# Performance work log

Measured on AMD Instinct MI355X. Metric: run time of the kernel, lower is better.

Reference implementation:

```python
import jax, jax.numpy as jnp
import numpy as np

H = 64       # hidden size hard-coded in the module
NH = 4       # n_heads
S = 500      # stock_num
D = 10       # num_day
T = 40       # num_text (news per day)
FP = 3       # price features
FT = 512     # text embedding dim


def gru_scan(x, Wih, Whh, bih, bhh):
    """Single-sequence GRU (torch gate convention). x: (T, F) -> hidden states (T, H)."""
    gi = x @ Wih + bih  # (T, 3H) precompute input gates outside the scan

    def step(h, g):
        gh = h @ Whh + bhh
        r = jax.nn.sigmoid(g[:H] + gh[:H])
        z = jax.nn.sigmoid(g[H:2 * H] + gh[H:2 * H])
        n = jnp.tanh(g[2 * H:] + r * gh[2 * H:])
        h_new = (1.0 - z) * n + z * h
        return h_new, h_new

    h0 = jnp.zeros((H,), x.dtype)
    _, hs = jax.lax.scan(step, h0, gi)
    return hs


def attn_pool(hs, W, v):
    """Additive attention pooling over time. hs: (T, H) -> (H,)."""
    scores = jnp.tanh(hs @ W) @ v          # (T,)
    alpha = jax.nn.softmax(scores)
    return alpha @ hs


def _gru_params(key, fin, scale=0.08):
    k1, k2, k3, k4 = jax.random.split(key, 4)
    return (jax.random.normal(k1, (S, fin, 3 * H)) * scale,
            jax.random.normal(k2, (S, H, 3 * H)) * scale,
            jax.random.normal(k3, (S, 3 * H)) * scale,
            jax.random.normal(k4, (S, 3 * H)) * scale)


def _attn_params(key, scale=0.08):
    k1, k2 = jax.random.split(key)
    return (jax.random.normal(k1, (S, H, H)) * scale,
            jax.random.normal(k2, (S, H)) * scale)


def setup_inputs() -> dict:
    key = jax.random.key(0)
    ks = jax.random.split(key, 20)
    inp = {}
    inp['text_input'] = jax.random.normal(ks[0], (S, D, T, FT), dtype=jnp.float32)
    inp['price_input'] = jax.random.normal(ks[1], (S, D, FP), dtype=jnp.float32)
    inp['label'] = jax.random.randint(ks[2], (S,), 0, 2)
    inp['adj'] = jnp.ones((S, S), dtype=jnp.float32)
    inp['train'] = 0
    # per-stock stacked parameters
    (inp['Wih_p'], inp['Whh_p'], inp['bih_p'], inp['bhh_p']) = _gru_params(ks[3], FP)
    (inp['Wa_p'], inp['va_p']) = _attn_params(ks[4])
    (inp['Wih_t'], inp['Whh_t'], inp['bih_t'], inp['bhh_t']) = _gru_params(ks[5], FT)
    (inp['Wa_t'], inp['va_t']) = _attn_params(ks[6])
    (inp['Wih_s'], inp['Whh_s'], inp['bih_s'], inp['bhh_s']) = _gru_params(ks[7], H)
    (inp['Wa_s'], inp['va_s']) = _attn_params(ks[8])
    inp['Wb'] = jax.random.normal(ks[9], (S, H, H, H)) * 0.05   # Bilinear weight (out,in1,in2)
    inp['bb'] = jax.random.normal(ks[10], (S, H)) * 0.05
    inp['Wbl'] = jax.random.normal(ks[11], (S, H, 2)) * 0.08
    inp['bbl'] = jax.random.normal(ks[12], (S, 2)) * 0.08
    # shared cross-stock self-attention projections and final fc
    inp['Wq'] = jax.random.normal(ks[13], (H, H)) * 0.08
    inp['bq'] = jax.random.normal(ks[14], (H,)) * 0.08
    inp['Wk'] = jax.random.normal(ks[15], (H, H)) * 0.08
    inp['bk'] = jax.random.normal(ks[16], (H,)) * 0.08
    inp['Wf'] = jax.random.normal(ks[17], (H, 2)) * 0.08
    inp['bf'] = jax.random.normal(ks[18], (2,)) * 0.08
    return inp


def _forward(text_input, price_input, label,
             Wih_p, Whh_p, bih_p, bhh_p, Wa_p, va_p,
             Wih_t, Whh_t, bih_t, bhh_t, Wa_t, va_t,
             Wih_s, Whh_s, bih_s, bhh_s, Wa_s, va_s,
             Wb, bb, Wbl, bbl, Wq, bq, Wk, bk, Wf, bf):
    # ---- per-stock price encoder: GRU over days + attention pooling ----
    def enc_price(x, a, b, c, d, W, v):
        return attn_pool(gru_scan(x, a, b, c, d), W, v)
    x_price = jax.vmap(enc_price)(price_input, Wih_p, Whh_p, bih_p, bhh_p, Wa_p, va_p)  # (S, H)

    # ---- per-stock, per-day text encoder ----
    def enc_text_stock(xdays, a, b, c, d, W, v):
        return jax.vmap(lambda x: attn_pool(gru_scan(x, a, b, c, d), W, v))(xdays)  # (D, H)
    news = jax.vmap(enc_text_stock)(text_input, Wih_t, Whh_t, bih_t, bhh_t, Wa_t, va_t)  # (S, D, H)

    # ---- per-stock sequence encoder over days ----
    text_vec = jax.vmap(enc_price)(news, Wih_s, Whh_s, bih_s, bhh_s, Wa_s, va_s)  # (S, H)

    # ---- bilinear fusion: tanh(Bilinear(text, price)) ----
    combined = jnp.tanh(jnp.einsum('si,skij,sj->sk', text_vec, Wb, x_price) + bb)  # (S, H)

    # ---- per-stock blending head ----
    out_1 = jnp.tanh(jnp.einsum('si,sik->sk', combined, Wbl) + bbl)  # (S, 2)

    # ---- cross-stock multi-head self-attention (q,k projected, v identity) ----
    dh = H // NH
    q = (combined @ Wq + bq).reshape(S, NH, dh)
    k = (combined @ Wk + bk).reshape(S, NH, dh)
    v = combined.reshape(S, NH, dh)
    scores = jnp.einsum('shd,thd->hst', q, k) / (dh ** 0.5)
    attn = jax.nn.softmax(scores, axis=-1)
    attn_out = jnp.einsum('hst,thd->shd', attn, v).reshape(S, H)

    x = jax.nn.elu(attn_out @ Wf + bf)  # (S, 2)
    output = jax.nn.softmax(x + out_1, axis=1)
    # faithful to the original: CrossEntropyLoss applied to already-softmaxed output
    logp = jax.nn.log_softmax(output, axis=1)
    loss = -jnp.mean(logp[jnp.arange(S), label])
    return loss, output


def reference(text_input, price_input, label, adj, train,
              Wih_p, Whh_p, bih_p, bhh_p, Wa_p, va_p,
              Wih_t, Whh_t, bih_t, bhh_t, Wa_t, va_t,
              Wih_s, Whh_s, bih_s, bhh_s, Wa_s, va_s,
              Wb, bb, Wbl, bbl, Wq, bq, Wk, bk, Wf, bf):
    return _forward(text_input, price_input, label,
                    Wih_p, Whh_p, bih_p, bhh_p, Wa_p, va_p,
                    Wih_t, Whh_t, bih_t, bhh_t, Wa_t, va_t,
                    Wih_s, Whh_s, bih_s, bhh_s, Wa_s, va_s,
                    Wb, bb, Wbl, bbl, Wq, bq, Wk, bk, Wf, bf)
```

## Files before the change

### kernel.cpp

```cpp
#include <hip/hip_runtime.h>

#define Sn 500
#define Dn 10
#define Tn 40
#define FPn 3
#define FTn 512
#define Hn 64
#define G3 192
#define NHn 4

typedef __attribute__((ext_vector_type(8))) short bf8_t;
typedef __attribute__((ext_vector_type(4))) float f4_t;

__device__ __forceinline__ unsigned short f2bf(float f) {
    union { float f; unsigned int u; } v; v.f = f;
    unsigned int r = v.u + 0x7fffu + ((v.u >> 16) & 1u);
    return (unsigned short)(r >> 16);
}
__device__ __forceinline__ float bflo(unsigned int u) {
    union { unsigned int u; float f; } v; v.u = u << 16; return v.f;
}
__device__ __forceinline__ float bfhi(unsigned int u) {
    union { unsigned int u; float f; } v; v.u = u & 0xffff0000u; return v.f;
}
__device__ __forceinline__ unsigned int cvtpk(float lo, float hi) {
    unsigned int r;
    asm("v_cvt_pk_bf16_f32 %0, %1, %2" : "=v"(r) : "v"(lo), "v"(hi));
    return r;
}
__device__ __forceinline__ float sigmoidf_(float x) { return 1.f / (1.f + __expf(-x)); }
__device__ __forceinline__ float tanhf_(float x) {
    x = fminf(15.f, fmaxf(-15.f, x));
    float e = __expf(2.f * x);
    return (e - 1.f) / (e + 1.f);
}
__device__ __forceinline__ float dot8(uint4 wv, f4_t hA, f4_t hB) {
    return bflo(wv.x) * hA[0] + bfhi(wv.x) * hA[1]
         + bflo(wv.y) * hA[2] + bfhi(wv.y) * hA[3]
         + bflo(wv.z) * hB[0] + bfhi(wv.z) * hB[1]
         + bflo(wv.w) * hB[2] + bfhi(wv.w) * hB[3];
}
union bfu { bf8_t v; unsigned int u[4]; };

__global__ __launch_bounds__(256, 2) void gi_gemm4(
    const float* __restrict__ text, const float* __restrict__ Wih,
    const float* __restrict__ bih, float* __restrict__ gi2)
{
    const int bid = blockIdx.x;
    const int xcd = bid & 7, ix = bid >> 3;
    const int swz = (xcd < 4 ? xcd * 313 : 4 * 313 + (xcd - 4) * 312) + ix;
    const int s = swz / 5, fi = swz % 5;
    const int tid = threadIdx.x, w = tid >> 6, l = tid & 63;
    const int lr = l & 15, kg = l >> 4;

    const float* Wihs = Wih + (size_t)s * FTn * G3 + w * 48 + lr;
    const float* xrow = text + ((size_t)s * 400 + fi * 80 + lr) * FTn + kg * 8;

    f4_t acc[5][3];
    #pragma unroll
    for (int a = 0; a < 5; a++)
        #pragma unroll
        for (int b = 0; b < 3; b++) acc[a][b] = (f4_t){0.f, 0.f, 0.f, 0.f};

    f4_t an0[5], an1[5];
    #pragma unroll
    for (int mt = 0; mt < 5; ++mt) {
        const float* p = xrow + (size_t)mt * 16 * FTn;
        an0[mt] = *(const f4_t*)p; an1[mt] = *(const f4_t*)(p + 4);
    }

    for (int kk = 0; kk < 16; ++kk) {
        bfu af[5];
        #pragma unroll
        for (int mt = 0; mt < 5; ++mt) {
            af[mt].u[0] = cvtpk(an0[mt][0], an0[mt][1]);
            af[mt].u[1] = cvtpk(an0[mt][2], an0[mt][3]);
            af[mt].u[2] = cvtpk(an1[mt][0], an1[mt][1]);
            af[mt].u[3] = cvtpk(an1[mt][2], an1[mt][3]);
        }
        if (kk < 15) {
            const float* px = xrow + (kk + 1) * 32;
            #pragma unroll
            for (int mt = 0; mt < 5; ++mt) {
                const float* p = px + (size_t)mt * 16 * FTn;
                an0[mt] = *(const f4_t*)p; an1[mt] = *(const f4_t*)(p + 4);
            }
        }
        bfu bfr[3];
        const float* bp0 = Wihs + (size_t)(kk * 32 + kg * 8) * G3;
        #pragma unroll
        for (int nc = 0; nc < 3; ++nc) {
            const float* bp = bp0 + nc * 16;
            float b0 = bp[0], b1 = bp[G3], b2 = bp[2 * G3], b3 = bp[3 * G3];
            float b4 = bp[4 * G3], b5 = bp[5 * G3], b6 = bp[6 * G3], b7 = bp[7 * G3];
            bfr[nc].u[0] = cvtpk(b0, b1); bfr[nc].u[1] = cvtpk(b2, b3);
            bfr[nc].u[2] = cvtpk(b4, b5); bfr[nc].u[3] = cvtpk(b6, b7);
        }
        #pragma unroll
        for (int mt = 0; mt < 5; ++mt)
            #pragma unroll
            for (int nc = 0; nc < 3; ++nc)
                acc[mt][nc] = __builtin_amdgcn_mfma_f32_16x16x32_bf16(af[mt].v, bfr[nc].v, acc[mt][nc], 0, 0, 0);
    }

    const float* bihs = bih + (size_t)s * G3 + w * 48 + lr;
    #pragma unroll
    for (int nc = 0; nc < 3; ++nc) {
        const int col = w * 48 + nc * 16 + lr;
        const float bv = bihs[nc * 16];
        #pragma unroll
        for (int mt = 0; mt < 5; ++mt)
            #pragma unroll
            for (int rg = 0; rg < 4; ++rg) {
                int r = mt * 16 + kg * 4 + rg;
                int hi = (r >= 40);
                int day = fi * 2 + hi;
                int t = r - hi * 40;
                gi2[((size_t)(s * 40 + t) * 10 + day) * 192 + col] = acc[mt][nc][rg] + bv;
            }
    }
}

__global__ __launch_bounds__(64, 1) void gru_text_f(
    const float* __restrict__ gi2, const float* __restrict__ Whh,
    const float* __restrict__ bhh, const float* __restrict__ Wa,
    const float* __restrict__ va, float* __restrict__ news)
{
    __shared__ __align__(16) float hrow[16 * 68];
    __shared__ __align__(16) unsigned char waT[Hn * 128];

    const int s = blockIdx.x, l = threadIdx.x;
    const int lr = l & 15, lg = l >> 4;

    const float* Whhs = Whh + (size_t)s * Hn * G3;
    bfu bwhh[2][12];
    #pragma unroll
    for (int ks = 0; ks < 2; ++ks)
        #pragma unroll
        for (int nt = 0; nt < 12; ++nt) {
            const float* p = Whhs + (size_t)(ks * 32 + lg * 8) * G3 + nt * 16 + lr;
            float b0 = p[0], b1 = p[G3], b2 = p[2 * G3], b3 = p[3 * G3];
            float b4 = p[4 * G3], b5 = p[5 * G3], b6 = p[6 * G3], b7 = p[7 * G3];
            bwhh[ks][nt].u[0] = cvtpk(b0, b1); bwhh[ks][nt].u[1] = cvtpk(b2, b3);
            bwhh[ks][nt].u[2] = cvtpk(b4, b5); bwhh[ks][nt].u[3] = cvtpk(b6, b7);
        }
    float bhh_l[12];
    #pragma unroll
    for (int nt = 0; nt < 12; ++nt) bhh_l[nt] = bhh[(size_t)s * G3 + nt * 16 + lr];
    float va_l[4];
    #pragma unroll
    for (int nt = 0; nt < 4; ++nt) va_l[nt] = va[(size_t)s * Hn + nt * 16 + lr];

    {
        const float* Was = Wa + (size_t)s * Hn * Hn;
        for (int r = 0; r < 64; ++r) {
            int e = l + r * 64, i = e >> 6, k = e & 63;
            *(unsigned short*)(waT + k * 128 + ((2 * i) ^ ((k & 7) << 4))) = f2bf(Was[e]);
        }
        #pragma unroll
        for (int r = 0; r < 17; ++r) hrow[l + r * 64] = 0.f;
    }
    __builtin_amdgcn_wave_barrier();

    int dayoff[4];
    #pragma unroll
    for (int rr = 0; rr < 4; ++rr) {
        int d = lg * 4 + rr; if (d > 9) d = 9;
        dayoff[rr] = d * 192 + lr;
    }
    const float* gbase = gi2 + (size_t)s * 40 * 1920;

    float val[48], valn[48];
    #pragma unroll
    for (int j = 0; j < 48; ++j) val[j] = gbase[dayoff[j & 3] + (j >> 2) * 16];

    bf8_t a0f, a1f;
    {   bfu z0; z0.u[0] = 0; z0.u[1] = 0; z0.u[2] = 0; z0.u[3] = 0; a0f = z0.v; a1f = z0.v; }

    float h[4][4], accv[4][4], den[4], m[4];
    #pragma unroll
    for (int nt = 0; nt < 4; ++nt)
        #pragma unroll
        for (int rr = 0; rr < 4; ++rr) { h[nt][rr] = 0.f; accv[nt][rr] = 0.f; }
    #pragma unroll
    for (int rr = 0; rr < 4; ++rr) { den[rr] = 0.f; m[rr] = -1e30f; }

    for (int t = 0; t < Tn; ++t) {
        f4_t acc[12];
        #pragma unroll
        for (int nt = 0; nt < 12; ++nt)
            acc[nt] = (f4_t){bhh_l[nt], bhh_l[nt], bhh_l[nt], bhh_l[nt]};
        #pragma unroll
        for (int nt = 0; nt < 12; ++nt) {
            acc[nt] = __builtin_amdgcn_mfma_f32_16x16x32_bf16(a0f, bwhh[0][nt].v, acc[nt], 0, 0, 0);
            acc[nt] = __builtin_amdgcn_mfma_f32_16x16x32_bf16(a1f, bwhh[1][nt].v, acc[nt], 0, 0, 0);
        }
        {
            const int tn = (t < Tn - 1) ? t + 1 : t;
            const float* gb = gbase + (size_t)tn * 1920;
            #pragma unroll
            for (int j = 0; j < 48; ++j) valn[j] = gb[dayoff[j & 3] + (j >> 2) * 16];
        }
        #pragma unroll
        for (int nt = 0; nt < 4; ++nt)
            #pragma unroll
            for (int rr = 0; rr < 4; ++rr) {
                float r = sigmoidf_(val[nt * 4 + rr] + acc[nt][rr]);
                float z = sigmoidf_(val[(nt + 4) * 4 + rr] + acc[nt + 4][rr]);
                float n = tanhf_(val[(nt + 8) * 4 + rr] + r * acc[nt + 8][rr]);
                h[nt][rr] = (1.f - z) * n + z * h[nt][rr];
            }
        __builtin_amdgcn_wave_barrier();
        #pragma unroll
        for (int rr = 0; rr < 4; ++rr) {
            int day = lg * 4 + rr;
            if (day < Dn) {
                #pragma unroll
                for (int nt = 0; nt < 4; ++nt) hrow[day * 68 + nt * 16 + lr] = h[nt][rr];
            }
        }
        __builtin_amdgcn_wave_barrier();
        {
            const float* hp = hrow + lr * 68 + lg * 8;
            f4_t x0 = *(const f4_t*)hp,        x1 = *(const f4_t*)(hp + 4);
            f4_t y0 = *(const f4_t*)(hp + 32), y1 = *(const f4_t*)(hp + 36);
            bfu t0, t1;
            t0.u[0] = cvtpk(x0[0], x0[1]); t0.u[1] = cvtpk(x0[2], x0[3]);
            t0.u[2] = cvtpk(x1[0], x1[1]); t0.u[3] = cvtpk(x1[2], x1[3]);
            t1.u[0] = cvtpk(y0[0], y0[1]); t1.u[1] = cvtpk(y0[2], y0[3]);
            t1.u[2] = cvtpk(y1[0], y1[1]); t1.u[3] = cvtpk(y1[2], y1[3]);
            a0f = t0.v; a1f = t1.v;
        }
        f4_t sc[4];
        #pragma unroll
        for (int nt = 0; nt < 4; ++nt) sc[nt] = (f4_t){0.f, 0.f, 0.f, 0.f};
        #pragma unroll
        for (int ks = 0; ks < 2; ++ks) {
            bf8_t av = ks ? a1f : a0f;
            #pragma unroll
            for (int nt = 0; nt < 4; ++nt) {
                bf8_t bwv = *(const bf8_t*)(waT + (nt * 16 + lr) * 128
                                            + ((ks * 64 + lg * 16) ^ ((lr & 7) << 4)));
                sc[nt] = __builtin_amdgcn_mfma_f32_16x16x32_bf16(av, bwv, sc[nt], 0, 0, 0);
            }
        }
        float pr[4];
        #pragma unroll
        for (int rr = 0; rr < 4; ++rr) {
            pr[rr] = tanhf_(sc[0][rr]) * va_l[0] + tanhf_(sc[1][rr]) * va_l[1]
                   + tanhf_(sc[2][rr]) * va_l[2] + tanhf_(sc[3][rr]) * va_l[3];
            pr[rr] += __shfl_xor(pr[rr], 1);
            pr[rr] += __shfl_xor(pr[rr], 2);
            pr[rr] += __shfl_xor(pr[rr], 4);
            pr[rr] += __shfl_xor(pr[rr], 8);
        }
        #pragma unroll
        for (int rr = 0; rr < 4; ++rr) {
            float mn = fmaxf(m[rr], pr[rr]);
            float s0 = __expf(m[rr] - mn);
            float p = __expf(pr[rr] - mn);
            den[rr] = den[rr] * s0 + p;
            #pragma unroll
            for (int nt = 0; nt < 4; ++nt)
                accv[nt][rr] = accv[nt][rr] * s0 + p * h[nt][rr];
            m[rr] = mn;
        }
        #pragma unroll
        for (int j = 0; j < 48; ++j) val[j] = valn[j];
    }
    #pragma unroll
    for (int rr = 0; rr < 4; ++rr) {
        int day = lg * 4 + rr;
        if (day < Dn) {
            float inv = 1.f / den[rr];
            #pragma unroll
            for (int nt = 0; nt < 4; ++nt)
                news[((size_t)s * Dn + day) * Hn + nt * 16 + lr] = accv[nt][rr] * inv;
        }
    }
}

__global__ __launch_bounds__(64, 1) void gru_small_f(
    const float* __restrict__ news,
    const float* __restrict__ Wih_s, const float* __restrict__ Whh_s,
    const float* __restrict__ bih_s, const float* __restrict__ bhh_s,
    const float* __restrict__ Wa_s, const float* __restrict__ va_s,
    const float* __restrict__ price, const float* __restrict__ Wih_p,
    const float* __restrict__ Whh_p, const float* __restrict__ bih_p,
    const float* __restrict__ bhh_p, const float* __restrict__ Wa_p,
    const float* __restrict__ va_p,
    float* __restrict__ tvec, float* __restrict__ xprice)
{
    __shared__ __align__(16) unsigned char sm[60928];
    unsigned char* whh2 = sm;
    unsigned char* wih2 = sm + 24576;
    unsigned char* wa2 = sm + 49152;
    float* newsL = (float*)(sm + 57600);
    float* hbuf  = (float*)(sm + 60320);
    float* priceL = (float*)(sm + 60608);

    const int s = blockIdx.x, l = threadIdx.x;

    {
        const float* W2 = Whh_s + (size_t)s * Hn * G3;
        const float* X2 = Wih_s + (size_t)s * Hn * G3;
        for (int r = 0; r < 192; ++r) {
            int e = l + r * 64, i = e / G3, j = e - i * G3;
            int off = j * 128 + ((2 * i) ^ ((j & 7) << 4));
            *(unsigned short*)(whh2 + off) = f2bf(W2[e]);
            *(unsigned short*)(wih2 + off) = f2bf(X2[e]);
        }
        const float* A2 = Wa_s + (size_t)s * Hn * Hn;
        for (int r = 0; r < 64; ++r) {
            int e = l + r * 64, i = e >> 6, k = e & 63;
            *(unsigned short*)(wa2 + k * 128 + ((2 * i) ^ ((k & 7) << 4))) = f2bf(A2[e]);
        }
        #pragma unroll
        for (int d = 0; d < Dn; ++d) newsL[d * 68 + l] = news[((size_t)s * Dn + d) * Hn + l];
        hbuf[l] = 0.f;
        if (l < 4) hbuf[64 + l] = 0.f;
    }
    __builtin_amdgcn_wave_barrier();
    {
        const float bi0 = bih_s[(size_t)s * G3 + l];
        const float bi1 = bih_s[(size_t)s * G3 + 64 + l];
        const float bi2 = bih_s[(size_t)s * G3 + 128 + l];
        const float bh0 = bhh_s[(size_t)s * G3 + l];
        const float bh1 = bhh_s[(size_t)s * G3 + 64 + l];
        const float bh2 = bhh_s[(size_t)s * G3 + 128 + l];
        const float vak = va_s[(size_t)s * Hn + l];
        const int swl = (l & 7) << 4;
        float h2 = 0.f, m2 = -1e30f, den2 = 0.f, av2 = 0.f;
        for (int t = 0; t < Dn; ++t) {
            float gh0 = bh0, gh1 = bh1, gh2 = bh2;
            float gg0 = bi0, gg1 = bi1, gg2 = bi2;
            #pragma unroll
            for (int ic = 0; ic < 8; ++ic) {
                const int off = (ic * 16) ^ swl;
                f4_t hA = *(const f4_t*)&hbuf[ic * 8];
                f4_t hB = *(const f4_t*)&hbuf[ic * 8 + 4];
                f4_t nA = *(const f4_t*)&newsL[t * 68 + ic * 8];
                f4_t nB = *(const f4_t*)&newsL[t * 68 + ic * 8 + 4];
                uint4 w0 = *(const uint4*)(whh2 + l * 128 + off);
                uint4 w1 = *(const uint4*)(whh2 + (l + 64) * 128 + off);
                uint4 w2 = *(const uint4*)(whh2 + (l + 128) * 128 + off);
                uint4 x0 = *(const uint4*)(wih2 + l * 128 + off);
                uint4 x1 = *(const uint4*)(wih2 + (l + 64) * 128 + off);
                uint4 x2 = *(const uint4*)(wih2 + (l + 128) * 128 + off);
                gh0 += dot8(w0, hA, hB); gh1 += dot8(w1, hA, hB); gh2 += dot8(w2, hA, hB);
                gg0 += dot8(x0, nA, nB); gg1 += dot8(x1, nA, nB); gg2 += dot8(x2, nA, nB);
            }
            float r = sigmoidf_(gg0 + gh0);
            float z = sigmoidf_(gg1 + gh1);
            float n = tanhf_(gg2 + r * gh2);
            h2 = (1.f - z) * n + z * h2;
            __builtin_amdgcn_wave_barrier();
            hbuf[l] = h2;
            __builtin_amdgcn_wave_barrier();
            float sk = 0.f;
            #pragma unroll
            for (int ic = 0; ic < 8; ++ic) {
                const int off = (ic * 16) ^ swl;
                uint4 wv = *(const uint4*)(wa2 + l * 128 + off);
                f4_t hA = *(const f4_t*)&hbuf[ic * 8];
                f4_t hB = *(const f4_t*)&hbuf[ic * 8 + 4];
                sk += dot8(wv, hA, hB);
            }
            float term = tanhf_(sk) * vak;
            #pragma unroll
            for (int off = 32; off; off >>= 1) term += __shfl_xor(term, off);
            float mn = fmaxf(m2, term);
            float s0 = __expf(m2 - mn);
            float p = __expf(term - mn);
            den2 = den2 * s0 + p;
            av2 = av2 * s0 + p * h2;
            m2 = mn;
        }
        tvec[(size_t)s * Hn + l] = av2 / den2;
    }
    __builtin_amdgcn_wave_barrier();

    {
        const float* W3 = Whh_p + (size_t)s * Hn * G3;
        for (int r = 0; r < 192; ++r) {
            int e = l + r * 64, i = e / G3, j = e - i * G3;
            *(unsigned short*)(whh2 + j * 128 + ((2 * i) ^ ((j & 7) << 4))) = f2bf(W3[e]);
        }
        const float* A3 = Wa_p + (size_t)s * Hn * Hn;
        for (int r = 0; r < 64; ++r) {
            int e = l + r * 64, i = e >> 6, k = e & 63;
            *(unsigned short*)(wa2 + k * 128 + ((2 * i) ^ ((k & 7) << 4))) = f2bf(A3[e]);
        }
        if (l < 30) priceL[l] = price[(size_t)s * 30 + l];
        hbuf[l] = 0.f;
        if (l < 4) hbuf[64 + l] = 0.f;
    }
    __builtin_amdgcn_wave_barrier();
    {
        float wp[3][3];
        #pragma unroll
        for (int i = 0; i < 3; ++i)
            #pragma unroll
            for (int g = 0; g < 3; ++g)
                wp[i][g] = Wih_p[(size_t)s * 3 * G3 + i * G3 + g * 64 + l];
        const float bi0 = bih_p[(size_t)s * G3 + l];
        const float bi1 = bih_p[(size_t)s * G3 + 64 + l];
        const float bi2 = bih_p[(size_t)s * G3 + 128 + l];
        const float bh0 = bhh_p[(size_t)s * G3 + l];
        const float bh1 = bhh_p[(size_t)s * G3 + 64 + l];
        const float bh2 = bhh_p[(size_t)s * G3 + 128 + l];
        const float vak = va_p[(size_t)s * Hn + l];
        const int swl = (l & 7) << 4;
        float h3 = 0.f, m3 = -1e30f, den3 = 0.f, av3 = 0.f;
        for (int t = 0; t < Dn; ++t) {
            float x0 = priceL[t * 3], x1 = priceL[t * 3 + 1], x2 = priceL[t * 3 + 2];
            float gg0 = bi0 + x0 * wp[0][0] + x1 * wp[1][0] + x2 * wp[2][0];
            float gg1 = bi1 + x0 * wp[0][1] + x1 * wp[1][1] + x2 * wp[2][1];
            float gg2 = bi2 + x0 * wp[0][2] + x1 * wp[1][2] + x2 * wp[2][2];
            float gh0 = bh0, gh1 = bh1, gh2 = bh2;
            #pragma unroll
            for (int ic = 0; ic < 8; ++ic) {
                const int off = (ic * 16) ^ swl;
                f4_t hA = *(const f4_t*)&hbuf[ic * 8];
                f4_t hB = *(const f4_t*)&hbuf[ic * 8 + 4];
                uint4 w0 = *(const uint4*)(whh2 + l * 128 + off);
                uint4 w1 = *(const uint4*)(whh2 + (l + 64) * 128 + off);
                uint4 w2 = *(const uint4*)(whh2 + (l + 128) * 128 + off);
                gh0 += dot8(w0, hA, hB); gh1 += dot8(w1, hA, hB); gh2 += dot8(w2, hA, hB);
            }
            float r = sigmoidf_(gg0 + gh0);
            float z = sigmoidf_(gg1 + gh1);
            float n = tanhf_(gg2 + r * gh2);
            h3 = (1.f - z) * n + z * h3;
            __builtin_amdgcn_wave_barrier();
            hbuf[l] = h3;
            __builtin_amdgcn_wave_barrier();
            float sk = 0.f;
            #pragma unroll
            for (int ic = 0; ic < 8; ++ic) {
                const int off = (ic * 16) ^ swl;
                uint4 wv = *(const uint4*)(wa2 + l * 128 + off);
                f4_t hA = *(const f4_t*)&hbuf[ic * 8];
                f4_t hB = *(const f4_t*)&hbuf[ic * 8 + 4];
                sk += dot8(wv, hA, hB);
            }
            float term = tanhf_(sk) * vak;
            #pragma unroll
            for (int off = 32; off; off >>= 1) term += __shfl_xor(term, off);
            float mn = fmaxf(m3, term);
            float s0 = __expf(m3 - mn);
            float p = __expf(term - mn);
            den3 = den3 * s0 + p;
            av3 = av3 * s0 + p * h3;
            m3 = mn;
        }
        xprice[(size_t)s * Hn + l] = av3 / den3;
    }
}

__global__ __launch_bounds__(256) void bilinear2(
    const float* __restrict__ Wb, const float* __restrict__ bb,
    const float* __restrict__ xprice, const float* __restrict__ tvec,
    float* __restrict__ combined)
{
    __shared__ __align__(16) float uT[Hn][32];
    __shared__ float tv[Hn];

    const int bid = blockIdx.x, s = bid >> 1, kh = bid & 1;
    const int tid = threadIdx.x;
    const int w = tid >> 6, l = tid & 63;
    if (tid < Hn) tv[tid] = tvec[s * Hn + tid];
    const int j4 = (l & 15) * 4;
    f4_t xq = *(const f4_t*)&xprice[s * Hn + j4];
    __syncthreads();

    const float* Wbs = Wb + (size_t)s * Hn * Hn * Hn;
    for (int g = 0; g < 128; ++g) {
        int P = kh * 2048 + w * 512 + g * 4 + (l >> 4);
        f4_t wv = *(const f4_t*)&Wbs[(size_t)P * Hn + j4];
        float dp = wv[0] * xq[0] + wv[1] * xq[1] + wv[2] * xq[2] + wv[3] * xq[3];
        dp += __shfl_xor(dp, 8);
        dp += __shfl_xor(dp, 4);
        dp += __shfl_xor(dp, 2);
        dp += __shfl_xor(dp, 1);
        if ((l & 15) == 0) { int k = P >> 6, i = P & 63; uT[i][k - kh * 32] = dp; }
    }
    __syncthreads();
    if (tid < 32) {
        const int k = kh * 32 + tid;
        float a = bb[s * Hn + k];
        for (int i = 0; i < Hn; i++) a += tv[i] * uT[i][tid];
        combined[s * Hn + k] = tanhf_(a);
    }
}

__global__ __launch_bounds__(64) void qk_proj(
    const float* __restrict__ combined, const float* __restrict__ Wq,
    const float* __restrict__ bq, const float* __restrict__ Wk,
    const float* __restrict__ bk, const float* __restrict__ Wbl,
    const float* __restrict__ bbl,
    float* __restrict__ qg, float* __restrict__ kg, float* __restrict__ out1)
{
    __shared__ float cl[Hn];
    const int s = blockIdx.x, l = threadIdx.x;
    cl[l] = combined[s * Hn + l];
    __syncthreads();
    float aq = bq[l], ak = bk[l];
    for (int i = 0; i < Hn; i++) {
        float ci = cl[i];
        aq += ci * Wq[i * Hn + l];
        ak += ci * Wk[i * Hn + l];
    }
    qg[s * Hn + l] = aq; kg[s * Hn + l] = ak;
    if (l < 2) {
        float a = bbl[s * 2 + l];
        for (int i = 0; i < Hn; i++) a += cl[i] * Wbl[(size_t)s * Hn * 2 + i * 2 + l];
        out1[s * 2 + l] = tanhf_(a);
    }
}

__global__ __launch_bounds__(256) void mhsa(
    const float* __restrict__ qg, const float* __restrict__ kg,
    const float* __restrict__ combined, const float* __restrict__ Wf,
    const float* __restrict__ bfp, const float* __restrict__ out1,
    float* __restrict__ dout)
{
    __shared__ __align__(16) float ql[Hn];
    __shared__ float sl[NHn][Sn];
    __shared__ float hsum[NHn];
    __shared__ float ao[Hn];
    __shared__ float red2[8];
    __shared__ float red3[4][Hn];

    const int sq = blockIdx.x, tid = threadIdx.x;
    if (tid < Hn) ql[tid] = qg[sq * Hn + tid];
    __syncthreads();

    for (int id = tid; id < Sn * NHn; id += 256) {
        int t = id >> 2, h = id & 3;
        const float* kp = &kg[t * Hn + h * 16];
        float a = 0.f;
        #pragma unroll
        for (int x = 0; x < 16; x += 4) {
            f4_t kv = *(const f4_t*)&kp[x];
            f4_t qv = *(const f4_t*)&ql[h * 16 + x];
            a += kv[0] * qv[0] + kv[1] * qv[1] + kv[2] * qv[2] + kv[3] * qv[3];
        }
        sl[h][t] = a * 0.25f;
    }
    __syncthreads();
    for (int h = 0; h < NHn; ++h) {
        float m = -1e30f;
        for (int t = tid; t < Sn; t += 256) m = fmaxf(m, sl[h][t]);
        for (int o = 32; o; o >>= 1) m = fmaxf(m, __shfl_xor(m, o));
        if ((tid & 63) == 0) red2[tid >> 6] = m;
        __syncthreads();
        m = fmaxf(fmaxf(red2[0], red2[1]), fmaxf(red2[2], red2[3]));
        float ps = 0.f;
        for (int t = tid; t < Sn; t += 256) { float p = __expf(sl[h][t] - m); sl[h][t] = p; ps += p; }
        for (int o = 32; o; o >>= 1) ps += __shfl_xor(ps, o);
        if ((tid & 63) == 0) red2[4 + (tid >> 6)] = ps;
        __syncthreads();
        if (tid == 0) hsum[h] = red2[4] + red2[5] + red2[6] + red2[7];
        __syncthreads();
    }
    {
        const int q = tid >> 6, j = tid & 63, h = j >> 4;
        float a = 0.f;
        for (int t = q * 125; t < q * 125 + 125; ++t) a += sl[h][t] * combined[t * Hn + j];
        red3[q][j] = a;
    }
    __syncthreads();
    if (tid < Hn)
        ao[tid] = (red3[0][tid] + red3[1][tid] + red3[2][tid] + red3[3][tid]) / hsum[tid >> 4];
    __syncthreads();
    if (tid == 0) {
        float l0 = bfp[0], l1 = bfp[1];
        for (int j = 0; j < Hn; j++) { float v = ao[j]; l0 += v * Wf[j * 2]; l1 += v * Wf[j * 2 + 1]; }
        l0 = l0 > 0.f ? l0 : __expf(l0) - 1.f;
        l1 = l1 > 0.f ? l1 : __expf(l1) - 1.f;
        l0 += out1[sq * 2]; l1 += out1[sq * 2 + 1];
        float m = fmaxf(l0, l1);
        float e0 = __expf(l0 - m), e1 = __expf(l1 - m);
        float inv = 1.f / (e0 + e1);
        dout[1 + sq * 2] = e0 * inv;
        dout[2 + sq * 2] = e1 * inv;
    }
}

__global__ __launch_bounds__(512) void loss_k(float* __restrict__ dout,
                                              const int* __restrict__ label)
{
    __shared__ float red[512];
    const int tid = threadIdx.x;
    float a = 0.f;
    if (tid < Sn) {
        float p0 = dout[1 + 2 * tid], p1 = dout[2 + 2 * tid];
        float m = fmaxf(p0, p1);
        float lse = m + __logf(__expf(p0 - m) + __expf(p1 - m));
        float pl = label[tid] ? p1 : p0;
        a = -(pl - lse);
    }
    red[tid] = a;
    __syncthreads();
    for (int o = 256; o; o >>= 1) {
        if (tid < o) red[tid] += red[tid + o];
        __syncthreads();
    }
    if (tid == 0) dout[0] = red[0] / (float)Sn;
}

extern "C" void kernel_launch(void* const* d_in, const int* in_sizes, int n_in,
                              void* d_out, int out_size, void* d_ws, size_t ws_size,
                              hipStream_t stream)
{
    const float* text  = (const float*)d_in[0];
    const float* price = (const float*)d_in[1];
    const int*   label = (const int*)  d_in[2];
    const float* Wih_p = (const float*)d_in[5];
    const float* Whh_p = (const float*)d_in[6];
    const float* bih_p = (const float*)d_in[7];
    const float* bhh_p = (const float*)d_in[8];
    const float* Wa_p  = (const float*)d_in[9];
    const float* va_p  = (const float*)d_in[10];
    const float* Wih_t = (const float*)d_in[11];
    const float* Whh_t = (const float*)d_in[12];
    const float* bih_t = (const float*)d_in[13];
    const float* bhh_t = (const float*)d_in[14];
    const float* Wa_t  = (const float*)d_in[15];
    const float* va_t  = (const float*)d_in[16];
    const float* Wih_s = (const float*)d_in[17];
    const float* Whh_s = (const float*)d_in[18];
    const float* bih_s = (const float*)d_in[19];
    const float* bhh_s = (const float*)d_in[20];
    const float* Wa_s  = (const float*)d_in[21];
    const float* va_s  = (const float*)d_in[22];
    const float* Wb    = (const float*)d_in[23];
    const float* bb    = (const float*)d_in[24];
    const float* Wbl   = (const float*)d_in[25];
    const float* bbl   = (const float*)d_in[26];
    const float* Wq    = (const float*)d_in[27];
    const float* bq    = (const float*)d_in[28];
    const float* Wk    = (const float*)d_in[29];
    const float* bk    = (const float*)d_in[30];
    const float* Wf    = (const float*)d_in[31];
    const float* bf_   = (const float*)d_in[32];

    float* ws = (float*)d_ws;
    float* news     = ws;
    float* xprice   = ws + 320000;
    float* tvec     = ws + 352000;
    float* combined = ws + 384000;
    float* qg       = ws + 416000;
    float* kg       = ws + 448000;
    float* out1     = ws + 480000;
    float* gi2      = ws + 481000;
    float* dout = (float*)d_out;

    gi_gemm4<<<Sn * 5, 256, 0, stream>>>(text, Wih_t, bih_t, gi2);
    gru_text_f<<<Sn, 64, 0, stream>>>(gi2, Whh_t, bhh_t, Wa_t, va_t, news);
    gru_small_f<<<Sn, 64, 0, stream>>>(news,
                                       Wih_s, Whh_s, bih_s, bhh_s, Wa_s, va_s,
                                       price, Wih_p, Whh_p, bih_p, bhh_p, Wa_p, va_p,
                                       tvec, xprice);
    bilinear2<<<Sn * 2, 256, 0, stream>>>(Wb, bb, xprice, tvec, combined);
    qk_proj<<<Sn, 64, 0, stream>>>(combined, Wq, bq, Wk, bk, Wbl, bbl, qg, kg, out1);
    mhsa<<<Sn, 256, 0, stream>>>(qg, kg, combined, Wf, bf_, out1, dout);
    loss_k<<<1, 512, 0, stream>>>(dout, label);
}
```

Before: 663.1 us.

## Pre-transpose Wih to bf16 and stage text tiles through shared memory

Adds a prep kernel that transposes each stock's text-GRU input weights and converts them to bf16, so the GEMM can load B fragments as contiguous 16-byte vectors instead of eight strided scalar loads per lane. The GEMM now stages the text activations in a double-buffered, XOR-swizzled LDS tile loaded with coalesced vector reads, and prefetches the next k-step while the MFMAs run. The bilinear kernel is split over four blocks per stock instead of two for more parallelism. The cost is an extra kernel launch and a full pass over the weights (read fp32, write bf16) every call, plus more LDS use and block barriers in the GEMM.

```diff
diff --git a/kernel.cpp b/kernel.cpp
--- a/kernel.cpp
+++ b/kernel.cpp
@@ -42,19 +42,73 @@
 }
 union bfu { bf8_t v; unsigned int u[4]; };
 
-__global__ __launch_bounds__(256, 2) void gi_gemm4(
-    const float* __restrict__ text, const float* __restrict__ Wih,
+__global__ __launch_bounds__(256) void wih_prep(
+    const float* __restrict__ Wih, unsigned short* __restrict__ wt)
+{
+    __shared__ float tile[64][65];
+    const int bid = blockIdx.x;
+    const int s = bid / 24, tlo = bid % 24;
+    const int kt = tlo / 3, ct = tlo % 3;
+    const int k0 = kt * 64, c0 = ct * 64;
+    const int tid = threadIdx.x;
+
+    const int c = tid & 63, r0 = tid >> 6;
+    const float* src = Wih + ((size_t)s * FTn + k0) * G3 + c0 + c;
+    #pragma unroll
+    for (int i = 0; i < 16; ++i) {
+        int r = i * 4 + r0;
+        tile[c][r] = src[(size_t)r * G3];
+    }
+    __syncthreads();
+
+    const int cl = tid >> 5, k2 = (tid & 31) * 2;
+    unsigned int* wout = (unsigned int*)(wt + ((size_t)s * G3 + c0) * FTn + k0);
+    #pragma unroll
+    for (int p = 0; p < 8; ++p) {
+        int col = cl + p * 8;
+        wout[col * 256 + (k2 >> 1)] = cvtpk(tile[col][k2], tile[col][k2 + 1]);
+    }
+}
+
+__global__ __launch_bounds__(256) void gi_gemm6(
+    const float* __restrict__ text, const unsigned short* __restrict__ wt,
     const float* __restrict__ bih, float* __restrict__ gi2)
 {
+    __shared__ __align__(16) float Ab[2][2560];
+
     const int bid = blockIdx.x;
     const int xcd = bid & 7, ix = bid >> 3;
-    const int swz = (xcd < 4 ? xcd * 313 : 4 * 313 + (xcd - 4) * 312) + ix;
+    const int swz = (xcd < 4 ? xcd * 313 : 1252 + (xcd - 4) * 312) + ix;
     const int s = swz / 5, fi = swz % 5;
     const int tid = threadIdx.x, w = tid >> 6, l = tid & 63;
     const int lr = l & 15, kg = l >> 4;
 
-    const float* Wihs = Wih + (size_t)s * FTn * G3 + w * 48 + lr;
-    const float* xrow = text + ((size_t)s * 400 + fi * 80 + lr) * FTn + kg * 8;
+    const float* xbase = text + ((size_t)s * 400 + fi * 80) * FTn;
+    const unsigned short* wtb = wt + ((size_t)s * G3 + w * 48) * FTn;
+
+    const int c0 = tid, c1 = tid + 256, c2 = tid + 512;
+
+    auto aload = [&](int kk, int c) -> f4_t {
+        int row = c >> 3, slot = c & 7;
+        return *(const f4_t*)(xbase + (size_t)row * FTn + kk * 32 + slot * 4);
+    };
+    auto awrite = [&](int c, f4_t v, float* buf) {
+        int row = c >> 3, slot = c & 7;
+        *(f4_t*)(buf + row * 32 + ((slot ^ (row & 7)) * 4)) = v;
+    };
+    auto afrag = [&](const float* buf, int mt) -> bf8_t {
+        int row = mt * 16 + lr;
+        int sw = row & 7;
+        f4_t x0 = *(const f4_t*)(buf + row * 32 + ((((kg << 1)) ^ sw) << 2));
+        f4_t x1 = *(const f4_t*)(buf + row * 32 + ((((kg << 1) | 1) ^ sw) << 2));
+        bfu t;
+        t.u[0] = cvtpk(x0[0], x0[1]); t.u[1] = cvtpk(x0[2], x0[3]);
+        t.u[2] = cvtpk(x1[0], x1[1]); t.u[3] = cvtpk(x1[2], x1[3]);
+        return t.v;
+    };
+    auto bload = [&](int kk, int nc) -> bf8_t {
+        return *(const bf8_t*)(wtb + (size_t)(nc * 16 + lr) * FTn + kk * 32 + kg * 8);
+    };
 
     f4_t acc[5][3];
     #pragma unroll
@@ -62,45 +116,35 @@
         #pragma unroll
         for (int b = 0; b < 3; b++) acc[a][b] = (f4_t){0.f, 0.f, 0.f, 0.f};
 
-    f4_t an0[5], an1[5];
-    #pragma unroll
-    for (int mt = 0; mt < 5; ++mt) {
-        const float* p = xrow + (size_t)mt * 16 * FTn;
-        an0[mt] = *(const f4_t*)p; an1[mt] = *(const f4_t*)(p + 4);
-    }
-
+    f4_t a0 = aload(0, c0), a1 = aload(0, c1), a2;
+    if (tid < 128) a2 = aload(0, c2);
+    bf8_t bc0 = bload(0, 0), bc1 = bload(0, 1), bc2 = bload(0, 2);
+    awrite(c0, a0, Ab[0]); awrite(c1, a1, Ab[0]);
+    if (tid < 128) awrite(c2, a2, Ab[0]);
+    __syncthreads();
+
+    bf8_t bn0 = bc0, bn1 = bc1, bn2 = bc2;
     for (int kk = 0; kk < 16; ++kk) {
-        bfu af[5];
+        float* cur = Ab[kk & 1];
+        float* nxt = Ab[(kk & 1) ^ 1];
+        if (kk < 15) {
+            a0 = aload(kk + 1, c0); a1 = aload(kk + 1, c1);
+            if (tid < 128) a2 = aload(kk + 1, c2);
+            bn0 = bload(kk + 1, 0); bn1 = bload(kk + 1, 1); bn2 = bload(kk + 1, 2);
+        }
         #pragma unroll
         for (int mt = 0; mt < 5; ++mt) {
-            af[mt].u[0] = cvtpk(an0[mt][0], an0[mt][1]);
-            af[mt].u[1] = cvtpk(an0[mt][2], an0[mt][3]);
-            af[mt].u[2] = cvtpk(an1[mt][0], an1[mt][1]);
-            af[mt].u[3] = cvtpk(an1[mt][2], an1[mt][3]);
+            bf8_t af = afrag(cur, mt);
+            acc[mt][0] = __builtin_amdgcn_mfma_f32_16x16x32_bf16(af, bc0, acc[mt][0], 0, 0, 0);
+            acc[mt][1] = __builtin_amdgcn_mfma_f32_16x16x32_bf16(af, bc1, acc[mt][1], 0, 0, 0);
+            acc[mt][2] = __builtin_amdgcn_mfma_f32_16x16x32_bf16(af, bc2, acc[mt][2], 0, 0, 0);
         }
         if (kk < 15) {
-            const float* px = xrow + (kk + 1) * 32;
-            #pragma unroll
-            for (int mt = 0; mt < 5; ++mt) {
-                const float* p = px + (size_t)mt * 16 * FTn;
-                an0[mt] = *(const f4_t*)p; an1[mt] = *(const f4_t*)(p + 4);
-            }
-        }
-        bfu bfr[3];
-        const float* bp0 = Wihs + (size_t)(kk * 32 + kg * 8) * G3;
-        #pragma unroll
-        for (int nc = 0; nc < 3; ++nc) {
-            const float* bp = bp0 + nc * 16;
-            float b0 = bp[0], b1 = bp[G3], b2 = bp[2 * G3], b3 = bp[3 * G3];
-            float b4 = bp[4 * G3], b5 = bp[5 * G3], b6 = bp[6 * G3], b7 = bp[7 * G3];
-            bfr[nc].u[0] = cvtpk(b0, b1); bfr[nc].u[1] = cvtpk(b2, b3);
-            bfr[nc].u[2] = cvtpk(b4, b5); bfr[nc].u[3] = cvtpk(b6, b7);
-        }
-        #pragma unroll
-        for (int mt = 0; mt < 5; ++mt)
-            #pragma unroll
-            for (int nc = 0; nc < 3; ++nc)
-                acc[mt][nc] = __builtin_amdgcn_mfma_f32_16x16x32_bf16(af[mt].v, bfr[nc].v, acc[mt][nc], 0, 0, 0);
+            awrite(c0, a0, nxt); awrite(c1, a1, nxt);
+            if (tid < 128) awrite(c2, a2, nxt);
+        }
+        __syncthreads();
+        bc0 = bn0; bc1 = bn1; bc2 = bn2;
     }
 
     const float* bihs = bih + (size_t)s * G3 + w * 48 + lr;
@@ -458,15 +502,15 @@
     }
 }
 
-__global__ __launch_bounds__(256) void bilinear2(
+__global__ __launch_bounds__(256) void bilinear4(
     const float* __restrict__ Wb, const float* __restrict__ bb,
     const float* __restrict__ xprice, const float* __restrict__ tvec,
     float* __restrict__ combined)
 {
-    __shared__ __align__(16) float uT[Hn][32];
+    __shared__ __align__(16) float uT[Hn][16];
     __shared__ float tv[Hn];
 
-    const int bid = blockIdx.x, s = bid >> 1, kh = bid & 1;
+    const int bid = blockIdx.x, s = bid >> 2, kq = bid & 3;
     const int tid = threadIdx.x;
     const int w = tid >> 6, l = tid & 63;
     if (tid < Hn) tv[tid] = tvec[s * Hn + tid];
@@ -475,19 +519,19 @@
     __syncthreads();
 
     const float* Wbs = Wb + (size_t)s * Hn * Hn * Hn;
-    for (int g = 0; g < 128; ++g) {
-        int P = kh * 2048 + w * 512 + g * 4 + (l >> 4);
+    for (int g = 0; g < 64; ++g) {
+        int P = kq * 1024 + w * 256 + g * 4 + (l >> 4);
         f4_t wv = *(const f4_t*)&Wbs[(size_t)P * Hn + j4];
         float dp = wv[0] * xq[0] + wv[1] * xq[1] + wv[2] * xq[2] + wv[3] * xq[3];
         dp += __shfl_xor(dp, 8);
         dp += __shfl_xor(dp, 4);
         dp += __shfl_xor(dp, 2);
         dp += __shfl_xor(dp, 1);
-        if ((l & 15) == 0) { int k = P >> 6, i = P & 63; uT[i][k - kh * 32] = dp; }
-    }
-    __syncthreads();
-    if (tid < 32) {
-        const int k = kh * 32 + tid;
+        if ((l & 15) == 0) { int k = P >> 6, i = P & 63; uT[i][k - kq * 16] = dp; }
+    }
+    __syncthreads();
+    if (tid < 16) {
+        const int k = kq * 16 + tid;
         float a = bb[s * Hn + k];
         for (int i = 0; i < Hn; i++) a += tv[i] * uT[i][tid];
         combined[s * Hn + k] = tanhf_(a);
@@ -655,15 +699,17 @@
     float* kg       = ws + 448000;
     float* out1     = ws + 480000;
     float* gi2      = ws + 481000;
+    unsigned short* wt = (unsigned short*)(ws + 481000 + 38400000);
     float* dout = (float*)d_out;
 
-    gi_gemm4<<<Sn * 5, 256, 0, stream>>>(text, Wih_t, bih_t, gi2);
+    wih_prep<<<Sn * 24, 256, 0, stream>>>(Wih_t, wt);
+    gi_gemm6<<<Sn * 5, 256, 0, stream>>>(text, wt, bih_t, gi2);
     gru_text_f<<<Sn, 64, 0, stream>>>(gi2, Whh_t, bhh_t, Wa_t, va_t, news);
     gru_small_f<<<Sn, 64, 0, stream>>>(news,
                                        Wih_s, Whh_s, bih_s, bhh_s, Wa_s, va_s,
                                        price, Wih_p, Whh_p, bih_p, bhh_p, Wa_p, va_p,
                                        tvec, xprice);
-    bilinear2<<<Sn * 2, 256, 0, stream>>>(Wb, bb, xprice, tvec, combined);
+    bilinear4<<<Sn * 4, 256, 0, stream>>>(Wb, bb, xprice, tvec, combined);
     qk_proj<<<Sn, 64, 0, stream>>>(combined, Wq, bq, Wk, bk, Wbl, bbl, qg, kg, out1);
     mhsa<<<Sn, 256, 0, stream>>>(qg, kg, combined, Wf, bf_, out1, dout);
     loss_k<<<1, 512, 0, stream>>>(dout, label);
```

New measurement: 644.6 us. 1.03x faster.
